# Optimization experiments

Measured on AMD Instinct MI355X. Metric: run time of the kernel, lower is better.

The kernel has to match this reference:

```python
import jax, jax.numpy as jnp
import numpy as np

D_MODEL = 256
N_HEADS = 8
N_LEVELS = 4
N_POINTS = 4
HEAD_DIM = D_MODEL // N_HEADS
SPATIAL = [(64, 64), (32, 32), (16, 16), (8, 8)]
LEN_IN = sum(h * w for h, w in SPATIAL)
BATCH = 4
LEN_Q = LEN_IN


def _offset_bias():
    # replicate the module's _reset_parameters grid init for sampling_offsets.bias
    th = np.arange(N_HEADS, dtype=np.float64) * (2.0 * np.pi / N_HEADS)
    g = np.stack([np.cos(th), np.sin(th)], -1)
    g = g / np.abs(g).max(-1, keepdims=True)
    g = np.tile(g[:, None, None, :], (1, N_LEVELS, N_POINTS, 1))
    g = g * (np.arange(N_POINTS) + 1)[None, None, :, None]
    return jnp.asarray(g.reshape(-1), jnp.float32)


def setup_inputs() -> dict:
    key = jax.random.key(0)
    ks = jax.random.split(key, 10)
    s = 1.0 / np.sqrt(D_MODEL)
    return {
        "query": jax.random.normal(ks[0], (BATCH, LEN_Q, D_MODEL), jnp.float32),
        "reference_points": jax.random.uniform(ks[1], (BATCH, LEN_Q, N_LEVELS, 2), jnp.float32),
        "input_flatten": jax.random.normal(ks[2], (BATCH, LEN_IN, D_MODEL), jnp.float32),
        "input_spatial_shapes": np.array(SPATIAL, dtype=np.int64),
        "input_level_start_index": np.cumsum([0] + [h * w for h, w in SPATIAL[:-1]]).astype(np.int64),
        "W_val": jax.random.normal(ks[3], (D_MODEL, D_MODEL), jnp.float32) * s,
        "b_val": jnp.zeros((D_MODEL,), jnp.float32),
        "W_off": jax.random.normal(ks[4], (D_MODEL, N_HEADS * N_LEVELS * N_POINTS * 2), jnp.float32) * 0.01,
        "b_off": _offset_bias(),
        "W_attn": jax.random.normal(ks[5], (D_MODEL, N_HEADS * N_LEVELS * N_POINTS), jnp.float32) * 0.01,
        "b_attn": jnp.zeros((N_HEADS * N_LEVELS * N_POINTS,), jnp.float32),
        "W_out": jax.random.normal(ks[6], (D_MODEL, D_MODEL), jnp.float32) * s,
        "b_out": jnp.zeros((D_MODEL,), jnp.float32),
    }


def bilinear_sample(v, grid):
    # v: [B, C, H, W]; grid: [B, Q, P, 2] normalized to [-1, 1] (x=W axis, y=H axis)
    # matches torch F.grid_sample(mode='bilinear', padding_mode='zeros', align_corners=False)
    B, C, H, W = v.shape
    x = (grid[..., 0] + 1.0) * (W * 0.5) - 0.5
    y = (grid[..., 1] + 1.0) * (H * 0.5) - 0.5
    x0 = jnp.floor(x)
    y0 = jnp.floor(y)
    wx = x - x0
    wy = y - y0
    v_flat = v.reshape(B, C, H * W)

    def corner(xi, yi, wgt):
        valid = (xi >= 0) & (xi <= W - 1) & (yi >= 0) & (yi <= H - 1)
        xc = jnp.clip(xi, 0, W - 1).astype(jnp.int32)
        yc = jnp.clip(yi, 0, H - 1).astype(jnp.int32)
        idx = (yc * W + xc).reshape(B, 1, -1)
        g = jnp.take_along_axis(v_flat, jnp.broadcast_to(idx, (B, C, idx.shape[-1])), axis=2)
        return g * (wgt * valid).reshape(B, 1, -1)

    out = (corner(x0, y0, (1 - wx) * (1 - wy))
           + corner(x0 + 1, y0, wx * (1 - wy))
           + corner(x0, y0 + 1, (1 - wx) * wy)
           + corner(x0 + 1, y0 + 1, wx * wy))
    return out.reshape(B, C, grid.shape[1], grid.shape[2])


def reference(query, reference_points, input_flatten, input_spatial_shapes,
              input_level_start_index, W_val, b_val, W_off, b_off,
              W_attn, b_attn, W_out, b_out):
    ss = np.asarray(input_spatial_shapes)  # static [L, 2] (H, W)
    Nb, Lq, _ = query.shape
    value = (input_flatten @ W_val + b_val).reshape(Nb, -1, N_HEADS, HEAD_DIM)
    off = (query @ W_off + b_off).reshape(Nb, Lq, N_HEADS, N_LEVELS, N_POINTS, 2)
    attn = (query @ W_attn + b_attn).reshape(Nb, Lq, N_HEADS, N_LEVELS * N_POINTS)
    attn = jax.nn.softmax(attn, -1).reshape(Nb, Lq, N_HEADS, N_LEVELS, N_POINTS)
    # offset normalizer: (W, H) per level
    normalizer = jnp.asarray(ss[:, ::-1].copy(), jnp.float32)
    loc = reference_points[:, :, None, :, None, :] + off / normalizer[None, None, None, :, None, :]
    grids = 2.0 * loc - 1.0  # [N, Lq, H, L, P, 2]
    splits = np.cumsum([int(h) * int(w) for h, w in ss])[:-1]
    value_list = jnp.split(value, splits, axis=1)
    out = jnp.zeros((Nb * N_HEADS, HEAD_DIM, Lq), query.dtype)
    for lid, (h, w) in enumerate(ss):
        h, w = int(h), int(w)
        v = value_list[lid].transpose(0, 2, 3, 1).reshape(Nb * N_HEADS, HEAD_DIM, h, w)
        g = grids[:, :, :, lid].transpose(0, 2, 1, 3, 4).reshape(Nb * N_HEADS, Lq, N_POINTS, 2)
        sampled = bilinear_sample(v, g)  # [N*H, D, Lq, P]
        aw = attn[:, :, :, lid].transpose(0, 2, 1, 3).reshape(Nb * N_HEADS, 1, Lq, N_POINTS)
        out = out + (sampled * aw).sum(-1)
    out = out.reshape(Nb, N_HEADS * HEAD_DIM, Lq).transpose(0, 2, 1)
    return out @ W_out + b_out
```

## Files before the change

### kernel.cpp

```cpp
#include <hip/hip_runtime.h>
#include <hip/hip_bf16.h>
#include <math.h>

typedef unsigned short ushort_t;
typedef __attribute__((ext_vector_type(8))) short bf16x8;
typedef __attribute__((ext_vector_type(4))) float f32x4;
typedef __attribute__((ext_vector_type(2))) float f32x2;

constexpr int BATCH   = 4;
constexpr int D_MODEL = 256;
constexpr int LEN_IN  = 5440;
constexpr int LEN_Q   = 5440;
constexpr int M_TOT   = BATCH * LEN_Q;

#define ASG __attribute__((address_space(1)))
#define ASL __attribute__((address_space(3)))

__device__ __forceinline__ void gld16(const void* g, void* l) {
    __builtin_amdgcn_global_load_lds((ASG const void*)g, (ASL void*)l, 16, 0, 0);
}

__device__ __forceinline__ ushort_t bfbits(float x) {
    __hip_bfloat16 h = __float2bfloat16(x);
    ushort_t u; __builtin_memcpy(&u, &h, 2); return u;
}
__device__ __forceinline__ unsigned pk2(float a, float b) {
    return (unsigned)bfbits(a) | ((unsigned)bfbits(b) << 16);
}

__global__ __launch_bounds__(256) void pack_weights(
    const float* __restrict__ Wv, const float* __restrict__ Wout,
    const float* __restrict__ Wo, const float* __restrict__ Wa,
    const float* __restrict__ b_off, const float* __restrict__ b_attn,
    ushort_t* __restrict__ wvT, ushort_t* __restrict__ woutT,
    ushort_t* __restrict__ woaT, float* __restrict__ bias_oa)
{
    const int blk = blockIdx.x, t = threadIdx.x;
    if (blk < 64) {
        const float* src = (blk < 32) ? Wv : Wout;
        ushort_t*    dst = (blk < 32) ? wvT : woutT;
        const int k0 = (blk & 31) * 8;
        float f[8];
#pragma unroll
        for (int i = 0; i < 8; i++) f[i] = src[(k0 + i) * 256 + t];
        *(uint4*)(dst + t * 256 + k0) =
            make_uint4(pk2(f[0], f[1]), pk2(f[2], f[3]),
                       pk2(f[4], f[5]), pk2(f[6], f[7]));
    } else if (blk < 96) {
        const int k0 = (blk - 64) * 8;
#pragma unroll
        for (int rep = 0; rep < 2; rep++) {
            const int j = (rep == 0) ? t : 256 + t;
            if (rep == 1 && t >= 128) break;
            float f[8];
#pragma unroll
            for (int i = 0; i < 8; i++)
                f[i] = (j < 256) ? Wo[(k0 + i) * 256 + j]
                                 : Wa[(k0 + i) * 128 + (j - 256)];
            *(uint4*)(woaT + j * 256 + k0) =
                make_uint4(pk2(f[0], f[1]), pk2(f[2], f[3]),
                           pk2(f[4], f[5]), pk2(f[6], f[7]));
        }
    } else {
        bias_oa[t] = b_off[t];
        if (t < 128) bias_oa[256 + t] = b_attn[t];
    }
}

template <int OUT_MODE, bool A_F32, int NB>
__device__ __forceinline__ void gemm_core(
    const void* __restrict__ Ap, const ushort_t* __restrict__ BT,
    const float* __restrict__ bias, void* __restrict__ Cp, int N,
    int bm, int bn, ushort_t* As, ushort_t* Bs)
{
    const int tid  = threadIdx.x;
    const int wave = tid >> 6, lane = tid & 63;
    const int wm = (wave >> 1) * 64, wn = (wave & 1) * 64;
    const int c0 = 2 * wave, c1 = 2 * wave + 1;
    const int kb = (lane & 3) * 8;
    const int ar0 = bm + c0 * 16 + (lane >> 2);
    const int ar1 = bm + c1 * 16 + (lane >> 2);
    const ushort_t* gA0h = nullptr; const ushort_t* gA1h = nullptr;
    const float*    gA0f = nullptr; const float*    gA1f = nullptr;
    if (A_F32) {
        gA0f = (const float*)Ap + (size_t)ar0 * 256 + kb;
        gA1f = (const float*)Ap + (size_t)ar1 * 256 + kb;
    } else {
        gA0h = (const ushort_t*)Ap + (size_t)ar0 * 256 + kb;
        gA1h = (const ushort_t*)Ap + (size_t)ar1 * 256 + kb;
    }
    const ushort_t* gB0[NB]; const ushort_t* gB1[NB];
#pragma unroll
    for (int nb = 0; nb < NB; nb++) {
        gB0[nb] = BT + (size_t)(bn + nb * 128 + c0 * 16 + (lane >> 2)) * 256 + kb;
        gB1[nb] = BT + (size_t)(bn + nb * 128 + c1 * 16 + (lane >> 2)) * 256 + kb;
    }

    auto STAGE = [&](int kt, int buf) {
        ushort_t* as = As + buf * 4096;
        ushort_t* bs = Bs + buf * (NB * 4096);
        if (A_F32) {
            const float* a0 = gA0f + kt * 32;
            const float* a1 = gA1f + kt * 32;
            float4 x0 = *(const float4*)a0;
            float4 x1 = *(const float4*)(a0 + 4);
            float4 y0 = *(const float4*)a1;
            float4 y1 = *(const float4*)(a1 + 4);
            *(uint4*)(as + c0 * 512 + lane * 8) =
                make_uint4(pk2(x0.x, x0.y), pk2(x0.z, x0.w),
                           pk2(x1.x, x1.y), pk2(x1.z, x1.w));
            *(uint4*)(as + c1 * 512 + lane * 8) =
                make_uint4(pk2(y0.x, y0.y), pk2(y0.z, y0.w),
                           pk2(y1.x, y1.y), pk2(y1.z, y1.w));
        } else {
            gld16(gA0h + kt * 32, as + c0 * 512);
            gld16(gA1h + kt * 32, as + c1 * 512);
        }
#pragma unroll
        for (int nb = 0; nb < NB; nb++) {
            gld16(gB0[nb] + kt * 32, bs + nb * 4096 + c0 * 512);
            gld16(gB1[nb] + kt * 32, bs + nb * 4096 + c1 * 512);
        }
    };

    f32x4 acc[NB][4][4] = {};
    const int row = lane & 15, kg = (lane >> 4) * 8;

    STAGE(0, 0);
    __syncthreads();

    for (int kt = 0; kt < 8; kt++) {
        const int cur = kt & 1;
        if (kt < 7) STAGE(kt + 1, cur ^ 1);
        const ushort_t* as = As + cur * 4096;
        const ushort_t* bs = Bs + cur * (NB * 4096);
        bf16x8 af[4];
#pragma unroll
        for (int i = 0; i < 4; i++)
            af[i] = *(const bf16x8*)(as + (wm + i * 16 + row) * 32 + kg);
#pragma unroll
        for (int nb = 0; nb < NB; nb++) {
            bf16x8 bfr[4];
#pragma unroll
            for (int j = 0; j < 4; j++)
                bfr[j] = *(const bf16x8*)(bs + nb * 4096 + (wn + j * 16 + row) * 32 + kg);
#pragma unroll
            for (int i = 0; i < 4; i++)
#pragma unroll
                for (int j = 0; j < 4; j++)
                    acc[nb][i][j] = __builtin_amdgcn_mfma_f32_16x16x32_bf16(
                        af[i], bfr[j], acc[nb][i][j], 0, 0, 0);
        }
        __syncthreads();
    }

    const int col = lane & 15, rbase = (lane >> 4) * 4;
#pragma unroll
    for (int nb = 0; nb < NB; nb++) {
#pragma unroll
        for (int j = 0; j < 4; j++) {
            const int cc = bn + nb * 128 + wn + j * 16 + col;
            const float bv = bias[cc];
#pragma unroll
            for (int i = 0; i < 4; i++) {
                const int rr = bm + wm + i * 16 + rbase;
#pragma unroll
                for (int r = 0; r < 4; r++) {
                    const float v = acc[nb][i][j][r] + bv;
                    const int m = rr + r;
                    if (OUT_MODE == 0) {
                        ((float*)Cp)[(size_t)m * N + cc] = v;
                    } else {
                        const int bb  = m / LEN_IN;
                        const int pix = m - bb * LEN_IN;
                        const int head = cc >> 5, ch = cc & 31;
                        ((ushort_t*)Cp)[((size_t)((bb * 8 + head) * LEN_IN + pix) << 5) + ch] = bfbits(v);
                    }
                }
            }
        }
    }
}

__global__ __launch_bounds__(256) void gemm_dual(
    const float* __restrict__ inflat, const ushort_t* __restrict__ wvT,
    const float* __restrict__ b_val, ushort_t* __restrict__ value_bf,
    const float* __restrict__ query, const ushort_t* __restrict__ woaT,
    const float* __restrict__ bias_oa, float* __restrict__ offattn)
{
    __shared__ ushort_t As[2 * 128 * 32];
    __shared__ ushort_t Bs[2 * 2 * 128 * 32];
    const int blk = blockIdx.x;
    if (blk < 170) {
        gemm_core<2, true, 2>(inflat, wvT, b_val, value_bf, 256,
                              blk * 128, 0, As, Bs);
    } else if (blk < 340) {
        gemm_core<0, true, 2>(query, woaT, bias_oa, offattn, 384,
                              (blk - 170) * 128, 0, As, Bs);
    } else {
        gemm_core<0, true, 1>(query, woaT, bias_oa, offattn, 384,
                              (blk - 340) * 128, 256, As, Bs);
    }
}

__global__ __launch_bounds__(256) void gemm_out(
    const ushort_t* __restrict__ mid_bf, const ushort_t* __restrict__ woutT,
    const float* __restrict__ b_out, float* __restrict__ out)
{
    __shared__ ushort_t As[2 * 128 * 32];
    __shared__ ushort_t Bs[2 * 128 * 32];
    const int bn = (blockIdx.x & 1) * 128, bm = (blockIdx.x >> 1) * 128;
    gemm_core<0, false, 1>(mid_bf, woutT, b_out, out, 256, bm, bn, As, Bs);
}

__device__ __forceinline__ void accd(f32x2& a, unsigned u, f32x2 w) {
    f32x2 v;
    v.x = __uint_as_float(u << 16);
    v.y = __uint_as_float(u & 0xFFFF0000u);
    a = w * v + a;
}
__device__ __forceinline__ void accp(f32x2* a, uint4 u, float wf) {
    const f32x2 w = {wf, wf};
    accd(a[0], u.x, w); accd(a[1], u.y, w);
    accd(a[2], u.z, w); accd(a[3], u.w, w);
}

__global__ __launch_bounds__(256) void msda_sample_v4(
    const ushort_t* __restrict__ value,
    const float* __restrict__ refp,
    const float* __restrict__ offattn,
    ushort_t* __restrict__ mid)
{
    __shared__ float4 wLDS[64][16];
    __shared__ int2   aLDS[64][16];
    __shared__ float  esLDS[64];

    const int tid = threadIdx.x;
    const unsigned bid = blockIdx.x;
    const int xcd   = bid & 7;
    const int pos   = bid >> 3;
    const int slice = pos / 85;
    const int qc    = pos - slice * 85;
    const int bh    = xcd * 4 + slice;
    const int b     = bh >> 3, h = bh & 7;
    const int bqbase = b * LEN_Q + qc * 64;

    {
        const int p  = tid & 15;
        const int qg = tid >> 4;
        const int l  = p >> 2;
        const int shift = 6 - l;
        const int W  = 1 << shift;
        const float fW   = (float)W;
        const float invW = __uint_as_float((unsigned)(127 - shift) << 23);
        const int st = (l == 0) ? 0 : (l == 1) ? 4096 : (l == 2) ? 5120 : 5376;

#pragma unroll
        for (int it = 0; it < 4; it++) {
            const int ql = it * 16 + qg;
            const int bq = bqbase + ql;
            const float* oab = offattn + (size_t)bq * 384;
            const float2 off = *(const float2*)(oab + h * 32 + p * 2);
            const float  lgv = oab[256 + h * 16 + p];
            const float2 rl  = *(const float2*)(refp + (size_t)bq * 8 + l * 2);

            float mx = lgv;
            mx = fmaxf(mx, __shfl_xor(mx, 1));
            mx = fmaxf(mx, __shfl_xor(mx, 2));
            mx = fmaxf(mx, __shfl_xor(mx, 4));
            mx = fmaxf(mx, __shfl_xor(mx, 8));
            const float e = __expf(lgv - mx);
            float es = e;
            es += __shfl_xor(es, 1);
            es += __shfl_xor(es, 2);
            es += __shfl_xor(es, 4);
            es += __shfl_xor(es, 8);

            const float x = (rl.x + off.x * invW) * fW - 0.5f;
            const float y = (rl.y + off.y * invW) * fW - 0.5f;
            const float x0f = floorf(x), y0f = floorf(y);
            const float wx = x - x0f, wy = y - y0f;
            const int ix0 = (int)x0f, iy0 = (int)y0f;
            const int ix1 = ix0 + 1,  iy1 = iy0 + 1;
            const float vx0 = (ix0 >= 0 && ix0 < W) ? 1.f : 0.f;
            const float vx1 = (ix1 >= 0 && ix1 < W) ? 1.f : 0.f;
            const float vy0 = (iy0 >= 0 && iy0 < W) ? 1.f : 0.f;
            const float vy1 = (iy1 >= 0 && iy1 < W) ? 1.f : 0.f;
            const int cx0 = min(max(ix0, 0), W - 1);
            const int cx1 = min(max(ix1, 0), W - 1);
            const int cy0 = min(max(iy0, 0), W - 1);
            const int cy1 = min(max(iy1, 0), W - 1);
            const float hx0 = (1.f - wx) * vx0, hx1 = wx * vx1;
            const float hy0 = (1.f - wy) * vy0, hy1 = wy * vy1;

            const int off00 = (st + (cy0 << shift) + cx0) << 6;
            const int dxB   = (cx1 - cx0) << 6;
            const int dyB   = ((cy1 - cy0) << shift) << 6;

            const int ps = p ^ (ql & 15);
            wLDS[ql][ps] = make_float4(e * hx0 * hy0, e * hx1 * hy0,
                                       e * hx0 * hy1, e * hx1 * hy1);
            aLDS[ql][ps] = make_int2(off00, (dxB << 16) | dyB);
            if (p == 0) esLDS[ql] = es;
        }
    }
    __syncthreads();

    const int ql = tid >> 2;
    const int cg = tid & 3;
    const int bq = bqbase + ql;
    const char* vb = (const char*)value + (size_t)bh * (LEN_IN * 64) + cg * 16;
    const float inv = 1.f / esLDS[ql];
    const int qs = ql & 15;

    f32x2 acc2[4];
#pragma unroll
    for (int d = 0; d < 4; d++) acc2[d] = (f32x2){0.f, 0.f};

#pragma unroll
    for (int pp = 0; pp < 16; pp++) {
        const float4 w  = wLDS[ql][pp ^ qs];
        const int2   ai = aLDS[ql][pp ^ qs];
        const int o00 = ai.x;
        const int dx  = ai.y >> 16;
        const int dy  = ai.y & 0xFFFF;
        const char* c00 = vb + o00;
        uint4 v00 = *(const uint4*)(c00);
        uint4 v01 = *(const uint4*)(c00 + dx);
        uint4 v10 = *(const uint4*)(c00 + dy);
        uint4 v11 = *(const uint4*)(c00 + dx + dy);
        accp(acc2, v00, w.x);
        accp(acc2, v01, w.y);
        accp(acc2, v10, w.z);
        accp(acc2, v11, w.w);
    }

    uint4 o;
    o.x = pk2(acc2[0].x * inv, acc2[0].y * inv);
    o.y = pk2(acc2[1].x * inv, acc2[1].y * inv);
    o.z = pk2(acc2[2].x * inv, acc2[2].y * inv);
    o.w = pk2(acc2[3].x * inv, acc2[3].y * inv);
    ((uint4*)(mid + (size_t)bq * 256 + h * 32))[cg] = o;
}

extern "C" void kernel_launch(void* const* d_in, const int* in_sizes, int n_in,
                              void* d_out, int out_size, void* d_ws, size_t ws_size,
                              hipStream_t stream)
{
    const float* query  = (const float*)d_in[0];
    const float* refp   = (const float*)d_in[1];
    const float* inflat = (const float*)d_in[2];
    const float* W_val  = (const float*)d_in[5];
    const float* b_val  = (const float*)d_in[6];
    const float* W_off  = (const float*)d_in[7];
    const float* W_attn = (const float*)d_in[9];
    const float* b_off  = (const float*)d_in[8];
    const float* b_attn = (const float*)d_in[10];
    const float* W_out  = (const float*)d_in[11];
    const float* b_out  = (const float*)d_in[12];
    float* out = (float*)d_out;

    char* ws = (char*)d_ws;
    ushort_t* mid_bf   = (ushort_t*)ws;
    ushort_t* value_bf = (ushort_t*)(ws + 11141120);
    ushort_t* wvT      = (ushort_t*)(ws + 22282240);
    ushort_t* woutT    = (ushort_t*)(ws + 22413312);
    ushort_t* woaT     = (ushort_t*)(ws + 22544384);
    float*    bias_oa  = (float*)   (ws + 22740992);
    float*    offattn  = (float*)   (ws + 22742528);

    dim3 blk(256);
    pack_weights<<<dim3(97), blk, 0, stream>>>(
        W_val, W_out, W_off, W_attn, b_off, b_attn,
        wvT, woutT, woaT, bias_oa);
    gemm_dual<<<dim3(510), blk, 0, stream>>>(
        inflat, wvT, b_val, value_bf, query, woaT, bias_oa, offattn);
    msda_sample_v4<<<dim3(2720), blk, 0, stream>>>(
        value_bf, refp, offattn, mid_bf);
    gemm_out<<<dim3(340), blk, 0, stream>>>(
        mid_bf, woutT, b_out, out);
}
```

Before: 176.0 us.

## Stage coarse value levels in LDS for bilinear sampling

Each block now copies the two smallest feature levels (16x16 and 8x8) of its batch-head value slice into a 20 KB LDS buffer using async global-to-LDS loads, with an XOR swizzle on the layout. Level start offsets for those levels are rebased to the LDS buffer, and the sampling loop is split so points of levels 0-1 still gather from global memory while levels 2-3 read their four bilinear corners from LDS. This aims to replace scattered global/L2 gathers on the small levels with cheaper LDS reads. The cost is a per-block bulk copy of 20 KB, repeated across thousands of blocks, plus higher LDS use per block that may lower occupancy.

```diff
diff --git a/kernel.cpp b/kernel.cpp
--- a/kernel.cpp
+++ b/kernel.cpp
@@ -224,8 +224,9 @@
     accd(a[0], u.x, w); accd(a[1], u.y, w);
     accd(a[2], u.z, w); accd(a[3], u.w, w);
 }
-
-__global__ __launch_bounds__(256) void msda_sample_v4(
+__device__ __forceinline__ int swz(int a) { return a ^ ((a >> 3) & 0x30); }
+
+__global__ __launch_bounds__(256) void msda_sample_v5(
     const ushort_t* __restrict__ value,
     const float* __restrict__ refp,
     const float* __restrict__ offattn,
@@ -234,8 +235,10 @@
     __shared__ float4 wLDS[64][16];
     __shared__ int2   aLDS[64][16];
     __shared__ float  esLDS[64];
+    __shared__ __align__(16) char vLDS[20480];
 
     const int tid = threadIdx.x;
+    const int wave = tid >> 6, lane = tid & 63;
     const unsigned bid = blockIdx.x;
     const int xcd   = bid & 7;
     const int pos   = bid >> 3;
@@ -246,6 +249,17 @@
     const int bqbase = b * LEN_Q + qc * 64;
 
     {
+        const char* sbase = (const char*)value + (size_t)bh * (LEN_IN * 64) + 5120 * 64;
+        char* ldst = vLDS + wave * 1024;
+        const int dl = wave * 1024 + lane * 16;
+#pragma unroll
+        for (int pass = 0; pass < 5; pass++) {
+            const int d = dl + pass * 4096;
+            gld16(sbase + swz(d), ldst + pass * 4096);
+        }
+    }
+
+    {
         const int p  = tid & 15;
         const int qg = tid >> 4;
         const int l  = p >> 2;
@@ -253,7 +267,7 @@
         const int W  = 1 << shift;
         const float fW   = (float)W;
         const float invW = __uint_as_float((unsigned)(127 - shift) << 23);
-        const int st = (l == 0) ? 0 : (l == 1) ? 4096 : (l == 2) ? 5120 : 5376;
+        const int st = (l == 0) ? 0 : (l == 1) ? 4096 : (l == 2) ? 0 : 256;
 
 #pragma unroll
         for (int it = 0; it < 4; it++) {
@@ -312,13 +326,14 @@
     const char* vb = (const char*)value + (size_t)bh * (LEN_IN * 64) + cg * 16;
     const float inv = 1.f / esLDS[ql];
     const int qs = ql & 15;
+    const int cg16 = cg * 16;
 
     f32x2 acc2[4];
 #pragma unroll
     for (int d = 0; d < 4; d++) acc2[d] = (f32x2){0.f, 0.f};
 
 #pragma unroll
-    for (int pp = 0; pp < 16; pp++) {
+    for (int pp = 0; pp < 8; pp++) {
         const float4 w  = wLDS[ql][pp ^ qs];
         const int2   ai = aLDS[ql][pp ^ qs];
         const int o00 = ai.x;
@@ -335,6 +350,26 @@
         accp(acc2, v11, w.w);
     }
 
+#pragma unroll
+    for (int pp = 8; pp < 16; pp++) {
+        const float4 w  = wLDS[ql][pp ^ qs];
+        const int2   ai = aLDS[ql][pp ^ qs];
+        const int dx  = ai.y >> 16;
+        const int dy  = ai.y & 0xFFFF;
+        const int r00 = ai.x + cg16;
+        const int r01 = r00 + dx;
+        const int r10 = r00 + dy;
+        const int r11 = r10 + dx;
+        uint4 v00 = *(const uint4*)(vLDS + swz(r00));
+        uint4 v01 = *(const uint4*)(vLDS + swz(r01));
+        uint4 v10 = *(const uint4*)(vLDS + swz(r10));
+        uint4 v11 = *(const uint4*)(vLDS + swz(r11));
+        accp(acc2, v00, w.x);
+        accp(acc2, v01, w.y);
+        accp(acc2, v10, w.z);
+        accp(acc2, v11, w.w);
+    }
+
     uint4 o;
     o.x = pk2(acc2[0].x * inv, acc2[0].y * inv);
     o.y = pk2(acc2[1].x * inv, acc2[1].y * inv);
@@ -375,7 +410,7 @@
         wvT, woutT, woaT, bias_oa);
     gemm_dual<<<dim3(510), blk, 0, stream>>>(
         inflat, wvT, b_val, value_bf, query, woaT, bias_oa, offattn);
-    msda_sample_v4<<<dim3(2720), blk, 0, stream>>>(
+    msda_sample_v5<<<dim3(2720), blk, 0, stream>>>(
         value_bf, refp, offattn, mid_bf);
     gemm_out<<<dim3(340), blk, 0, stream>>>(
         mid_bf, woutT, b_out, out);
```

Result: slower. 179.8 us (+2.2%).
